# Optimization experiments

Measured on AMD Instinct MI355X. Metric: run time of the kernel, lower is better.

Reference implementation:

```python
import jax, jax.numpy as jnp
import numpy as np

GAMMA = 0.5
BATCH, DIM, UNITS = 16384, 512, 1024


def setup_inputs() -> dict:
    key = jax.random.key(0)
    k1, k2 = jax.random.split(key)
    inputs = jax.random.normal(k1, (BATCH, DIM), dtype=jnp.float32)
    mu = jax.random.normal(k2, (DIM, UNITS), dtype=jnp.float32)
    return {"inputs": inputs, "mu": mu}


def reference(inputs, mu):
    # Squared L2 distance from each input row to each center (column of mu):
    x_sq = jnp.sum(inputs * inputs, axis=1, keepdims=True)        # [B, 1]
    mu_sq = jnp.sum(mu * mu, axis=0, keepdims=True)               # [1, U]
    cross = inputs @ mu                                           # [B, U] GEMM
    l2 = x_sq - 2.0 * cross + mu_sq                                # [B, U]
    return jnp.exp(-GAMMA * l2)
```

## Files before the change

kernel.cpp:

```cpp
#include <hip/hip_runtime.h>

#define BATCH 16384
#define DIM   512
#define UNITS 1024

typedef float v16f __attribute__((ext_vector_type(16)));

#define MFMA(a, b, c) __builtin_amdgcn_mfma_f32_32x32x16_fp8_fp8((a), (b), (c), 0, 0, 0)

__global__ __launch_bounds__(1024, 4)
void rbf_fused_kernel(const float* __restrict__ in, const float* __restrict__ mu,
                      float* __restrict__ out) {
    __shared__ __attribute__((aligned(16))) unsigned char smem[155648];
    unsigned char* Bs = smem;
    unsigned char* As = smem + 131072;
    float* xsq_red  = (float*)(smem + 147456);
    float* musq_red = (float*)(smem + 151552);
    float* xsq_l    = (float*)(smem + 153600);
    float* musq_l   = (float*)(smem + 154624);

    const int t  = threadIdx.x;
    const int l  = t & 63;
    const int w  = t >> 6;
    const int ln = l & 31;
    const int h  = l >> 5;

    const int b   = blockIdx.x;
    const int xcd = b & 7;
    const int j   = b >> 3;
    const int m0  = (xcd * 8 + (j & 7)) * 256;
    const int n0  = (j >> 3) * 256;
    const int wm  = (w >> 2) * 64;
    const int wn  = (w & 3) * 64;

    const int ar = t >> 2, ap = t & 3;
    const float* arow = in + (size_t)(m0 + ar) * DIM + ap * 8;
    const int aidx = ((((ar >> 5) * 2 + (ap >> 1)) * 64) + (ap & 1) * 32 + (ar & 31)) * 8;

    float4 g0 = *(const float4*)(arow + 0);
    float4 g1 = *(const float4*)(arow + 4);

    {
        const int ng  = w >> 1;
        const int kwb = (w & 1) * 16;
        const float* msrc = mu + (size_t)(kwb * 16 + h * 8) * UNITS + n0 + ng * 32 + ln;
        unsigned char* bdst = Bs + ((ng * 32 + kwb) * 64 + l) * 8;
        float s = 0.f;
#pragma unroll 4
        for (int kk = 0; kk < 16; kk++) {
            float v[8];
#pragma unroll
            for (int jj = 0; jj < 8; jj++) v[jj] = msrc[(size_t)(kk * 16 + jj) * UNITS];
#pragma unroll
            for (int jj = 0; jj < 8; jj++) s += v[jj] * v[jj];
            int lo = __builtin_amdgcn_cvt_pk_fp8_f32(v[0], v[1], 0, false);
            lo     = __builtin_amdgcn_cvt_pk_fp8_f32(v[2], v[3], lo, true);
            int hi = __builtin_amdgcn_cvt_pk_fp8_f32(v[4], v[5], 0, false);
            hi     = __builtin_amdgcn_cvt_pk_fp8_f32(v[6], v[7], hi, true);
            *(int2*)(bdst + kk * 512) = make_int2(lo, hi);
        }
        s += __shfl_xor(s, 32, 64);
        if (h == 0) musq_red[(ng * 32 + ln) * 2 + (w & 1)] = s;
    }

    float sA = g0.x * g0.x + g0.y * g0.y + g0.z * g0.z + g0.w * g0.w
             + g1.x * g1.x + g1.y * g1.y + g1.z * g1.z + g1.w * g1.w;
    {
        int lo = __builtin_amdgcn_cvt_pk_fp8_f32(g0.x, g0.y, 0, false);
        lo     = __builtin_amdgcn_cvt_pk_fp8_f32(g0.z, g0.w, lo, true);
        int hi = __builtin_amdgcn_cvt_pk_fp8_f32(g1.x, g1.y, 0, false);
        hi     = __builtin_amdgcn_cvt_pk_fp8_f32(g1.z, g1.w, hi, true);
        *(int2*)(As + aidx) = make_int2(lo, hi);
    }
    __syncthreads();
    if (t < 256) musq_l[t] = -0.5f * (musq_red[t * 2] + musq_red[t * 2 + 1]);

    const long* BsL = (const long*)Bs;
    v16f acc[2][2];
#pragma unroll
    for (int c = 0; c < 2; c++)
#pragma unroll
        for (int g = 0; g < 2; g++) acc[c][g] = (v16f)0.f;

#pragma unroll 2
    for (int i = 0; i < 16; i++) {
        float4 f0, f1;
        if (i < 15) {
            f0 = *(const float4*)(arow + (i + 1) * 32);
            f1 = *(const float4*)(arow + (i + 1) * 32 + 4);
        }
        const long* AsL = (const long*)(As + (i & 1) * 8192);
        long a[2][2], bb[2][2];
#pragma unroll
        for (int c = 0; c < 2; c++)
#pragma unroll
            for (int kh = 0; kh < 2; kh++)
                a[c][kh] = AsL[(((w >> 2) * 2 + c) * 2 + kh) * 64 + l];
#pragma unroll
        for (int g = 0; g < 2; g++)
#pragma unroll
            for (int kh = 0; kh < 2; kh++)
                bb[g][kh] = BsL[(((w & 3) * 2 + g) * 32 + 2 * i + kh) * 64 + l];
#pragma unroll
        for (int kh = 0; kh < 2; kh++) {
            acc[0][0] = MFMA(a[0][kh], bb[0][kh], acc[0][0]);
            acc[0][1] = MFMA(a[0][kh], bb[1][kh], acc[0][1]);
            acc[1][0] = MFMA(a[1][kh], bb[0][kh], acc[1][0]);
            acc[1][1] = MFMA(a[1][kh], bb[1][kh], acc[1][1]);
        }
        if (i < 15) {
            sA += f0.x * f0.x + f0.y * f0.y + f0.z * f0.z + f0.w * f0.w
                + f1.x * f1.x + f1.y * f1.y + f1.z * f1.z + f1.w * f1.w;
            int lo = __builtin_amdgcn_cvt_pk_fp8_f32(f0.x, f0.y, 0, false);
            lo     = __builtin_amdgcn_cvt_pk_fp8_f32(f0.z, f0.w, lo, true);
            int hi = __builtin_amdgcn_cvt_pk_fp8_f32(f1.x, f1.y, 0, false);
            hi     = __builtin_amdgcn_cvt_pk_fp8_f32(f1.z, f1.w, hi, true);
            *(int2*)(As + ((i + 1) & 1) * 8192 + aidx) = make_int2(lo, hi);
        }
        __syncthreads();
    }

    xsq_red[ar * 4 + ap] = sA;
    __syncthreads();
    if (t < 256)
        xsq_l[t] = -0.5f * (xsq_red[t * 4] + xsq_red[t * 4 + 1]
                          + xsq_red[t * 4 + 2] + xsq_red[t * 4 + 3]);
    __syncthreads();

#pragma unroll
    for (int c = 0; c < 2; c++) {
        const size_t mrow = m0 + wm + c * 32;
#pragma unroll
        for (int g = 0; g < 2; g++) {
            const int nc = n0 + wn + g * 32;
            const float mb = musq_l[wn + g * 32 + ln];
#pragma unroll
            for (int r = 0; r < 16; r++) {
                const int rl = (r & 3) + 8 * (r >> 2) + 4 * h;
                const float xb = xsq_l[wm + c * 32 + rl];
                float v = __expf(acc[c][g][r] + xb + mb);
                __builtin_nontemporal_store(
                    v, out + (mrow + rl) * UNITS + nc + ln);
            }
        }
    }
}

extern "C" void kernel_launch(void* const* d_in, const int* in_sizes, int n_in,
                              void* d_out, int out_size, void* d_ws, size_t ws_size,
                              hipStream_t stream) {
    const float* inputs = (const float*)d_in[0];
    const float* mu     = (const float*)d_in[1];
    float* out = (float*)d_out;
    (void)d_ws; (void)ws_size;

    rbf_fused_kernel<<<256, 1024, 0, stream>>>(inputs, mu, out);
}
```

Measured before the change: 117.4 us.

## Halve block N-tile to 128, use 512-thread blocks with 16-wide K steps

Each block now covers a 256x128 output tile with 8 waves instead of 256x256 with 16 waves, and the grid doubles to 512 blocks. LDS drops to about 75 KB, which should let more blocks share a CU and help occupancy and balance across CUs. The A tile is streamed in 16-wide K chunks over 32 iterations with a two-deep register prefetch. The cost is twice as many barriers per block, and each A row is loaded and converted to fp8 twice across the grid.

```diff
diff --git a/kernel.cpp b/kernel.cpp
--- a/kernel.cpp
+++ b/kernel.cpp
@@ -5,19 +5,30 @@
 #define UNITS 1024
 
 typedef float v16f __attribute__((ext_vector_type(16)));
+#define MFMA_F8(a, b, c) __builtin_amdgcn_mfma_f32_32x32x16_fp8_fp8((a), (b), (c), 0, 0, 0)
 
-#define MFMA(a, b, c) __builtin_amdgcn_mfma_f32_32x32x16_fp8_fp8((a), (b), (c), 0, 0, 0)
+__device__ __forceinline__ int2 cvt8(const float4 f0, const float4 f1) {
+    int lo = __builtin_amdgcn_cvt_pk_fp8_f32(f0.x, f0.y, 0, false);
+    lo     = __builtin_amdgcn_cvt_pk_fp8_f32(f0.z, f0.w, lo, true);
+    int hi = __builtin_amdgcn_cvt_pk_fp8_f32(f1.x, f1.y, 0, false);
+    hi     = __builtin_amdgcn_cvt_pk_fp8_f32(f1.z, f1.w, hi, true);
+    return make_int2(lo, hi);
+}
+__device__ __forceinline__ float dot8(const float4 f0, const float4 f1) {
+    return f0.x * f0.x + f0.y * f0.y + f0.z * f0.z + f0.w * f0.w
+         + f1.x * f1.x + f1.y * f1.y + f1.z * f1.z + f1.w * f1.w;
+}
 
-__global__ __launch_bounds__(1024, 4)
+__global__ __launch_bounds__(512, 4)
 void rbf_fused_kernel(const float* __restrict__ in, const float* __restrict__ mu,
                       float* __restrict__ out) {
-    __shared__ __attribute__((aligned(16))) unsigned char smem[155648];
+    __shared__ __attribute__((aligned(16))) unsigned char smem[75264];
     unsigned char* Bs = smem;
-    unsigned char* As = smem + 131072;
-    float* xsq_red  = (float*)(smem + 147456);
-    float* musq_red = (float*)(smem + 151552);
-    float* xsq_l    = (float*)(smem + 153600);
-    float* musq_l   = (float*)(smem + 154624);
+    unsigned char* As = smem + 65536;
+    float* musq_red = (float*)(smem + 73728);
+    float* musq_l   = (float*)(smem + 74752);
+    float* xsq_red  = (float*)smem;
+    float* xsq_l    = (float*)(smem + 2048);
 
     const int t  = threadIdx.x;
     const int l  = t & 63;
@@ -29,22 +40,25 @@
     const int xcd = b & 7;
     const int j   = b >> 3;
     const int m0  = (xcd * 8 + (j & 7)) * 256;
-    const int n0  = (j >> 3) * 256;
-    const int wm  = (w >> 2) * 64;
-    const int wn  = (w & 3) * 64;
+    const int n0  = (j >> 3) * 128;
+    const int wm  = (w >> 1) * 64;
+    const int wn  = (w & 1) * 64;
 
-    const int ar = t >> 2, ap = t & 3;
-    const float* arow = in + (size_t)(m0 + ar) * DIM + ap * 8;
-    const int aidx = ((((ar >> 5) * 2 + (ap >> 1)) * 64) + (ap & 1) * 32 + (ar & 31)) * 8;
+    const int ar = t >> 1, seg = t & 1;
+    const float* arow = in + (size_t)(m0 + ar) * DIM + seg * 8;
+    const int aidx = (((ar >> 5) * 64) + seg * 32 + (ar & 31)) * 8;
 
-    float4 g0 = *(const float4*)(arow + 0);
-    float4 g1 = *(const float4*)(arow + 4);
+    float4 ga[2][2];
+    ga[0][0] = ((const float4*)arow)[0];
+    ga[0][1] = ((const float4*)arow)[1];
+    ga[1][0] = ((const float4*)(arow + 16))[0];
+    ga[1][1] = ((const float4*)(arow + 16))[1];
 
     {
         const int ng  = w >> 1;
         const int kwb = (w & 1) * 16;
         const float* msrc = mu + (size_t)(kwb * 16 + h * 8) * UNITS + n0 + ng * 32 + ln;
-        unsigned char* bdst = Bs + ((ng * 32 + kwb) * 64 + l) * 8;
+        unsigned char* bdst = Bs + (((ng * 32 + kwb) * 64) + l) * 8;
         float s = 0.f;
 #pragma unroll 4
         for (int kk = 0; kk < 16; kk++) {
@@ -63,17 +77,10 @@
         if (h == 0) musq_red[(ng * 32 + ln) * 2 + (w & 1)] = s;
     }
 
-    float sA = g0.x * g0.x + g0.y * g0.y + g0.z * g0.z + g0.w * g0.w
-             + g1.x * g1.x + g1.y * g1.y + g1.z * g1.z + g1.w * g1.w;
-    {
-        int lo = __builtin_amdgcn_cvt_pk_fp8_f32(g0.x, g0.y, 0, false);
-        lo     = __builtin_amdgcn_cvt_pk_fp8_f32(g0.z, g0.w, lo, true);
-        int hi = __builtin_amdgcn_cvt_pk_fp8_f32(g1.x, g1.y, 0, false);
-        hi     = __builtin_amdgcn_cvt_pk_fp8_f32(g1.z, g1.w, hi, true);
-        *(int2*)(As + aidx) = make_int2(lo, hi);
-    }
+    float sA = dot8(ga[0][0], ga[0][1]);
+    *(int2*)(As + aidx) = cvt8(ga[0][0], ga[0][1]);
     __syncthreads();
-    if (t < 256) musq_l[t] = -0.5f * (musq_red[t * 2] + musq_red[t * 2 + 1]);
+    if (t < 128) musq_l[t] = -0.5f * (musq_red[t * 2] + musq_red[t * 2 + 1]);
 
     const long* BsL = (const long*)Bs;
     v16f acc[2][2];
@@ -83,48 +90,32 @@
         for (int g = 0; g < 2; g++) acc[c][g] = (v16f)0.f;
 
 #pragma unroll 2
-    for (int i = 0; i < 16; i++) {
-        float4 f0, f1;
-        if (i < 15) {
-            f0 = *(const float4*)(arow + (i + 1) * 32);
-            f1 = *(const float4*)(arow + (i + 1) * 32 + 4);
+    for (int i = 0; i < 32; i++) {
+        if (i < 30) {
+            ga[i & 1][0] = ((const float4*)(arow + (i + 2) * 16))[0];
+            ga[i & 1][1] = ((const float4*)(arow + (i + 2) * 16))[1];
         }
-        const long* AsL = (const long*)(As + (i & 1) * 8192);
-        long a[2][2], bb[2][2];
-#pragma unroll
-        for (int c = 0; c < 2; c++)
-#pragma unroll
-            for (int kh = 0; kh < 2; kh++)
-                a[c][kh] = AsL[(((w >> 2) * 2 + c) * 2 + kh) * 64 + l];
-#pragma unroll
-        for (int g = 0; g < 2; g++)
-#pragma unroll
-            for (int kh = 0; kh < 2; kh++)
-                bb[g][kh] = BsL[(((w & 3) * 2 + g) * 32 + 2 * i + kh) * 64 + l];
-#pragma unroll
-        for (int kh = 0; kh < 2; kh++) {
-            acc[0][0] = MFMA(a[0][kh], bb[0][kh], acc[0][0]);
-            acc[0][1] = MFMA(a[0][kh], bb[1][kh], acc[0][1]);
-            acc[1][0] = MFMA(a[1][kh], bb[0][kh], acc[1][0]);
-            acc[1][1] = MFMA(a[1][kh], bb[1][kh], acc[1][1]);
-        }
-        if (i < 15) {
-            sA += f0.x * f0.x + f0.y * f0.y + f0.z * f0.z + f0.w * f0.w
-                + f1.x * f1.x + f1.y * f1.y + f1.z * f1.z + f1.w * f1.w;
-            int lo = __builtin_amdgcn_cvt_pk_fp8_f32(f0.x, f0.y, 0, false);
-            lo     = __builtin_amdgcn_cvt_pk_fp8_f32(f0.z, f0.w, lo, true);
-            int hi = __builtin_amdgcn_cvt_pk_fp8_f32(f1.x, f1.y, 0, false);
-            hi     = __builtin_amdgcn_cvt_pk_fp8_f32(f1.z, f1.w, hi, true);
-            *(int2*)(As + ((i + 1) & 1) * 8192 + aidx) = make_int2(lo, hi);
+        const long* AsL = (const long*)(As + (i & 1) * 4096);
+        long a0 = AsL[((w >> 1) * 2 + 0) * 64 + l];
+        long a1 = AsL[((w >> 1) * 2 + 1) * 64 + l];
+        long b0 = BsL[(((w & 1) * 2 + 0) * 32 + i) * 64 + l];
+        long b1 = BsL[(((w & 1) * 2 + 1) * 32 + i) * 64 + l];
+        acc[0][0] = MFMA_F8(a0, b0, acc[0][0]);
+        acc[0][1] = MFMA_F8(a0, b1, acc[0][1]);
+        acc[1][0] = MFMA_F8(a1, b0, acc[1][0]);
+        acc[1][1] = MFMA_F8(a1, b1, acc[1][1]);
+        if (i < 31) {
+            sA += dot8(ga[(i + 1) & 1][0], ga[(i + 1) & 1][1]);
+            *(int2*)(As + ((i + 1) & 1) * 4096 + aidx)
+                = cvt8(ga[(i + 1) & 1][0], ga[(i + 1) & 1][1]);
         }
         __syncthreads();
     }
 
-    xsq_red[ar * 4 + ap] = sA;
+    xsq_red[ar * 2 + seg] = sA;
     __syncthreads();
     if (t < 256)
-        xsq_l[t] = -0.5f * (xsq_red[t * 4] + xsq_red[t * 4 + 1]
-                          + xsq_red[t * 4 + 2] + xsq_red[t * 4 + 3]);
+        xsq_l[t] = -0.5f * (xsq_red[t * 2] + xsq_red[t * 2 + 1]);
     __syncthreads();
 
 #pragma unroll
@@ -154,5 +145,5 @@
     float* out = (float*)d_out;
     (void)d_ws; (void)ws_size;
 
-    rbf_fused_kernel<<<256, 1024, 0, stream>>>(inputs, mu, out);
+    rbf_fused_kernel<<<512, 512, 0, stream>>>(inputs, mu, out);
 }
```

New measurement: 122.6 us. 4.5% more time.
